# Optimization experiments

Measured on AMD Instinct MI355X. Metric: run time of the kernel, lower is better.

## Reference

```python
import jax, jax.numpy as jnp
import numpy as np

SMOOTH_SIZE = 3      # config.smooth_size (p); window = 2p+1
KERN_LAM = 0.003     # config.kern_lam
# config.kern_smooth = True, config.kern_squash = True, p_dropout = 0 (identity)


def _smooth(k, p):
    # k: (C, L). Reflect-pad then moving average with window 2p+1 (conv1d with ones/W).
    w = 2 * p + 1
    kp = jnp.pad(k, ((0, 0), (p, p)), mode="reflect")            # (C, L+2p)
    smooth_w = jnp.ones((1, 1, w), dtype=k.dtype) / w            # (out=1, in=1, W)
    out = jax.lax.conv_general_dilated(kp[:, None, :], smooth_w,
                                       window_strides=(1,), padding="VALID")
    return out[:, 0, :]                                          # (C, L)


def _squash(k, lam):
    # soft-threshold: relu(|k| - lam) * sign(k)
    return jax.nn.relu(jnp.abs(k) - lam) * jnp.sign(k)


def _fftconv(x, k):
    # x: (B, C, L), k: (C, L) -> causal-ish linear conv via zero-padded FFT, truncated to L
    L = x.shape[-1]
    xf = jnp.fft.rfft(x, n=2 * L)                                # (B, C, L+1) complex
    kf = jnp.fft.rfft(k, n=2 * L)                                # (C, L+1) complex, broadcasts
    return jnp.fft.irfft(xf * kf, n=2 * L)[..., :L]              # (B, C, L)


def setup_inputs() -> dict:
    key = jax.random.key(0)
    kx, kk = jax.random.split(key)
    x = jax.random.normal(kx, (8, 256, 8192), dtype=jnp.float32)
    kern = jax.random.normal(kk, (256, 8192), dtype=jnp.float32) * 0.02
    return {"x": x, "kern": kern}


def reference(x, kern):
    k = _smooth(kern, SMOOTH_SIZE)
    k = _squash(k, KERN_LAM)
    # dropout with p=0 is identity
    return _fftconv(x, k)
```

## Files before the change

kernel.cpp:

```cpp
#include <hip/hip_runtime.h>
#include <math.h>

#define L_SEQ    8192
#define NFFT     8192
#define LOG2N    13
#define NTHREADS 512
#define NB       8
#define NC       256
#define PI_F     3.14159265358979323846f

__device__ __forceinline__ float2 cmul(float2 a, float2 b) {
    return make_float2(fmaf(a.x, b.x, -(a.y * b.y)), fmaf(a.x, b.y, a.y * b.x));
}
__device__ __forceinline__ float2 cadd(float2 a, float2 b) { return make_float2(a.x + b.x, a.y + b.y); }
__device__ __forceinline__ float2 csub(float2 a, float2 b) { return make_float2(a.x - b.x, a.y - b.y); }
__device__ __forceinline__ float2 conj2(float2 a) { return make_float2(a.x, -a.y); }
__device__ __forceinline__ int brev13(unsigned x) { return (int)(__brev(x) >> (32 - LOG2N)); }

__device__ __forceinline__ void fft_dif(float2* z, const int tid) {
    for (int m = NFFT / 2; m >= 1; m >>= 1) {
        __syncthreads();
        const float ang = -PI_F / (float)m;
        #pragma unroll
        for (int r = 0; r < (NFFT / 2) / NTHREADS; ++r) {
            const int k  = r * NTHREADS + tid;
            const int j  = k & (m - 1);
            const int i0 = 2 * k - j;
            const int i1 = i0 + m;
            const float2 a = z[i0];
            const float2 b = z[i1];
            float s, cc;
            __sincosf(ang * (float)j, &s, &cc);
            z[i0] = cadd(a, b);
            z[i1] = cmul(csub(a, b), make_float2(cc, s));
        }
    }
    __syncthreads();
}

__device__ __forceinline__ void fft_dit_inv(float2* z, const int tid) {
    for (int m = 1; m <= NFFT / 2; m <<= 1) {
        __syncthreads();
        const float ang = PI_F / (float)m;
        #pragma unroll
        for (int r = 0; r < (NFFT / 2) / NTHREADS; ++r) {
            const int k  = r * NTHREADS + tid;
            const int j  = k & (m - 1);
            const int i0 = 2 * k - j;
            const int i1 = i0 + m;
            const float2 a = z[i0];
            float s, cc;
            __sincosf(ang * (float)j, &s, &cc);
            const float2 b = cmul(z[i1], make_float2(cc, s));
            z[i0] = cadd(a, b);
            z[i1] = csub(a, b);
        }
    }
    __syncthreads();
}

__global__ __launch_bounds__(NTHREADS)
void fftconv_kernel(const float* __restrict__ x,
                    const float* __restrict__ kern,
                    float* __restrict__ out) {
    extern __shared__ float2 z[];
    const int tid = threadIdx.x;
    const int c   = blockIdx.x >> 1;
    const int bh  = blockIdx.x & 1;

    {
        const float* kr = kern + (size_t)c * L_SEQ;
        const int base = tid * 16;
        float v[16];
        #pragma unroll
        for (int e = 0; e < 16; ++e) {
            const int i = base + e;
            float s = 0.f;
            #pragma unroll
            for (int d = -3; d <= 3; ++d) {
                int idx = i + d;
                idx = (idx < 0) ? -idx : idx;
                idx = (idx >= L_SEQ) ? (2 * L_SEQ - 2 - idx) : idx;
                s += kr[idx];
            }
            s *= (1.0f / 7.0f);
            const float a = fabsf(s) - 0.003f;
            v[e] = (a > 0.f) ? copysignf(a, s) : 0.f;
        }
        #pragma unroll
        for (int e = 0; e < 8; ++e)
            z[tid * 8 + e] = make_float2(v[2 * e], v[2 * e + 1]);
        #pragma unroll
        for (int r = 0; r < 8; ++r)
            z[NFFT / 2 + r * NTHREADS + tid] = make_float2(0.f, 0.f);
    }
    fft_dif(z, tid);

    float2 kA[9], kB[9];
    #pragma unroll
    for (int it = 0; it < 9; ++it) {
        const int f = tid + it * NTHREADS;
        if (f <= NFFT / 2) {
            const int g = (NFFT - f) & (NFFT - 1);
            const float2 Zf = z[brev13(f)];
            const float2 Zg = z[brev13(g)];
            float s, cc;
            __sincosf(PI_F * (float)f * (1.0f / NFFT), &s, &cc);
            const float2 E = make_float2(0.5f * (Zf.x + Zg.x), 0.5f * (Zf.y - Zg.y));
            const float2 O = make_float2(0.5f * (Zf.y + Zg.y), -0.5f * (Zf.x - Zg.x));
            kA[it] = cadd(E, cmul(make_float2(cc, -s), O));
            kB[it] = cadd(conj2(E), cmul(make_float2(-cc, -s), conj2(O)));
        }
    }

    for (int bi = 0; bi < 4; ++bi) {
        const int b = bh * 4 + bi;
        __syncthreads();
        const float2* xr = (const float2*)(x + ((size_t)b * NC + c) * L_SEQ);
        #pragma unroll
        for (int r = 0; r < 8; ++r)
            z[r * NTHREADS + tid] = xr[r * NTHREADS + tid];
        #pragma unroll
        for (int r = 0; r < 8; ++r)
            z[NFFT / 2 + r * NTHREADS + tid] = make_float2(0.f, 0.f);

        fft_dif(z, tid);

        #pragma unroll
        for (int it = 0; it < 9; ++it) {
            const int f = tid + it * NTHREADS;
            if (f <= NFFT / 2) {
                const int g  = (NFFT - f) & (NFFT - 1);
                const int pf = brev13(f), pg = brev13(g);
                const float2 Zf = z[pf];
                const float2 Zg = z[pg];
                float s, cc;
                __sincosf(PI_F * (float)f * (1.0f / NFFT), &s, &cc);
                const float2 E = make_float2(0.5f * (Zf.x + Zg.x), 0.5f * (Zf.y - Zg.y));
                const float2 O = make_float2(0.5f * (Zf.y + Zg.y), -0.5f * (Zf.x - Zg.x));
                const float2 Xf = cadd(E, cmul(make_float2(cc, -s), O));
                const float2 Xg = cadd(conj2(E), cmul(make_float2(-cc, -s), conj2(O)));
                float2 Yf = cmul(Xf, kA[it]);
                float2 Yg = cmul(Xg, kB[it]);
                Yf = make_float2(Yf.x * (1.0f / NFFT), Yf.y * (1.0f / NFFT));
                Yg = make_float2(Yg.x * (1.0f / NFFT), Yg.y * (1.0f / NFFT));
                const float2 P = make_float2(0.5f * (Yf.x + Yg.x), 0.5f * (Yf.y - Yg.y));
                const float2 Q = make_float2(0.5f * (Yf.x - Yg.x), 0.5f * (Yf.y + Yg.y));
                z[pf] = cadd(P, cmul(make_float2(-s, cc), Q));
                if (f != 0) {
                    const float2 Pg = make_float2(P.x, -P.y);
                    const float2 Qg = make_float2(-Q.x, Q.y);
                    z[pg] = cadd(Pg, cmul(make_float2(-s, -cc), Qg));
                }
            }
        }

        fft_dit_inv(z, tid);

        float2* orow = (float2*)(out + ((size_t)b * NC + c) * L_SEQ);
        #pragma unroll
        for (int r = 0; r < 8; ++r)
            orow[r * NTHREADS + tid] = z[r * NTHREADS + tid];
    }
}

extern "C" void kernel_launch(void* const* d_in, const int* in_sizes, int n_in,
                              void* d_out, int out_size, void* d_ws, size_t ws_size,
                              hipStream_t stream) {
    const float* x    = (const float*)d_in[0];
    const float* kern = (const float*)d_in[1];
    float* out        = (float*)d_out;
    const size_t lds_bytes = (size_t)NFFT * sizeof(float2);
    hipLaunchKernelGGL(fftconv_kernel, dim3(NC * 2), dim3(NTHREADS), lds_bytes, stream,
                       x, kern, out);
}
```

Measured before the change: 378.0 us.

## Replace radix-2 shared-memory FFT with register radix-16 stages and swizzled LDS

Replaces the 13-stage radix-2 LDS FFT, which needs a barrier and a sincos for every stage, with a few register-resident radix-16 passes (16x16x16x2 decomposition). Twiddles come from one sincos per pass plus complex multiplies, LDS indices are XOR-swizzled to avoid bank conflicts, and the last radix-2 step uses cross-lane shuffles. The zero-padded half of the input and the discarded half of the output are skipped in the first and last passes, and the kernel smoothing uses a running sum. Register pressure rises (launch bounds ask for 4 blocks) and the recursive twiddle multiplication may cost some accuracy.

```diff
diff --git a/kernel.cpp b/kernel.cpp
--- a/kernel.cpp
+++ b/kernel.cpp
@@ -1,166 +1,286 @@
 #include <hip/hip_runtime.h>
 #include <math.h>
 
-#define L_SEQ    8192
-#define NFFT     8192
-#define LOG2N    13
-#define NTHREADS 512
-#define NB       8
-#define NC       256
-#define PI_F     3.14159265358979323846f
-
-__device__ __forceinline__ float2 cmul(float2 a, float2 b) {
-    return make_float2(fmaf(a.x, b.x, -(a.y * b.y)), fmaf(a.x, b.y, a.y * b.x));
-}
-__device__ __forceinline__ float2 cadd(float2 a, float2 b) { return make_float2(a.x + b.x, a.y + b.y); }
-__device__ __forceinline__ float2 csub(float2 a, float2 b) { return make_float2(a.x - b.x, a.y - b.y); }
-__device__ __forceinline__ float2 conj2(float2 a) { return make_float2(a.x, -a.y); }
-__device__ __forceinline__ int brev13(unsigned x) { return (int)(__brev(x) >> (32 - LOG2N)); }
-
-__device__ __forceinline__ void fft_dif(float2* z, const int tid) {
-    for (int m = NFFT / 2; m >= 1; m >>= 1) {
-        __syncthreads();
-        const float ang = -PI_F / (float)m;
-        #pragma unroll
-        for (int r = 0; r < (NFFT / 2) / NTHREADS; ++r) {
-            const int k  = r * NTHREADS + tid;
-            const int j  = k & (m - 1);
-            const int i0 = 2 * k - j;
-            const int i1 = i0 + m;
-            const float2 a = z[i0];
-            const float2 b = z[i1];
-            float s, cc;
-            __sincosf(ang * (float)j, &s, &cc);
-            z[i0] = cadd(a, b);
-            z[i1] = cmul(csub(a, b), make_float2(cc, s));
-        }
-    }
-    __syncthreads();
-}
-
-__device__ __forceinline__ void fft_dit_inv(float2* z, const int tid) {
-    for (int m = 1; m <= NFFT / 2; m <<= 1) {
-        __syncthreads();
-        const float ang = PI_F / (float)m;
-        #pragma unroll
-        for (int r = 0; r < (NFFT / 2) / NTHREADS; ++r) {
-            const int k  = r * NTHREADS + tid;
-            const int j  = k & (m - 1);
-            const int i0 = 2 * k - j;
-            const int i1 = i0 + m;
-            const float2 a = z[i0];
-            float s, cc;
-            __sincosf(ang * (float)j, &s, &cc);
-            const float2 b = cmul(z[i1], make_float2(cc, s));
-            z[i0] = cadd(a, b);
-            z[i1] = csub(a, b);
-        }
-    }
-    __syncthreads();
-}
-
-__global__ __launch_bounds__(NTHREADS)
+#define NFFT  8192
+#define L_SEQ 8192
+#define NC    256
+#define NTH   512
+
+typedef float2 cplx;
+
+__device__ __forceinline__ cplx cmul(cplx a, cplx b){
+    return make_float2(fmaf(a.x,b.x,-(a.y*b.y)), fmaf(a.x,b.y,a.y*b.x));
+}
+__device__ __forceinline__ cplx cadd(cplx a, cplx b){ return make_float2(a.x+b.x,a.y+b.y); }
+__device__ __forceinline__ cplx csub(cplx a, cplx b){ return make_float2(a.x-b.x,a.y-b.y); }
+__device__ __forceinline__ int swz(int e){ return e ^ ((e>>4)&15); }
+
+#define C16f 0.9238795325112867f
+#define S16f 0.3826834323650898f
+#define RH   0.7071067811865476f
+#define PI2F 6.28318530717958647692f
+
+template<bool INV>
+__device__ __forceinline__ void radix4(cplx& A0, cplx& A1, cplx& A2, cplx& A3){
+    cplx t0=cadd(A0,A2), t1=csub(A0,A2), t2=cadd(A1,A3), t3=csub(A1,A3);
+    A0=cadd(t0,t2); A2=csub(t0,t2);
+    if(!INV){ A1=make_float2(t1.x+t3.y,t1.y-t3.x); A3=make_float2(t1.x-t3.y,t1.y+t3.x); }
+    else    { A1=make_float2(t1.x-t3.y,t1.y+t3.x); A3=make_float2(t1.x+t3.y,t1.y-t3.x); }
+}
+template<bool INV>
+__device__ __forceinline__ cplx twid(cplx v, float re, float im){
+    return INV ? cmul(v, make_float2(re,  im)) : cmul(v, make_float2(re, -im));
+}
+template<bool INV>
+__device__ __forceinline__ cplx mulmi(cplx v){
+    return INV ? make_float2(-v.y, v.x) : make_float2(v.y, -v.x);
+}
+
+template<bool INV>
+__device__ __forceinline__ void dft16_tail(cplx b[4][4], cplx v[16]){
+    b[1][1]=twid<INV>(b[1][1],C16f,S16f);
+    b[1][2]=twid<INV>(b[1][2],RH,RH);
+    b[1][3]=twid<INV>(b[1][3],S16f,C16f);
+    b[2][1]=twid<INV>(b[2][1],RH,RH);
+    b[2][2]=mulmi<INV>(b[2][2]);
+    b[2][3]=twid<INV>(b[2][3],-RH,RH);
+    b[3][1]=twid<INV>(b[3][1],S16f,C16f);
+    b[3][2]=twid<INV>(b[3][2],-RH,RH);
+    b[3][3]=twid<INV>(b[3][3],-C16f,-S16f);
+    #pragma unroll
+    for(int k0=0;k0<4;k0++){
+        radix4<INV>(b[0][k0],b[1][k0],b[2][k0],b[3][k0]);
+        v[k0]=b[0][k0]; v[k0+4]=b[1][k0]; v[k0+8]=b[2][k0]; v[k0+12]=b[3][k0];
+    }
+}
+template<bool INV>
+__device__ __forceinline__ void dft16(cplx v[16]){
+    cplx b[4][4];
+    #pragma unroll
+    for(int n0=0;n0<4;n0++){
+        b[n0][0]=v[n0]; b[n0][1]=v[n0+4]; b[n0][2]=v[n0+8]; b[n0][3]=v[n0+12];
+        radix4<INV>(b[n0][0],b[n0][1],b[n0][2],b[n0][3]);
+    }
+    dft16_tail<INV>(b, v);
+}
+__device__ __forceinline__ void dft16_half(cplx v[16]){
+    cplx b[4][4];
+    #pragma unroll
+    for(int n0=0;n0<4;n0++){
+        cplx a=v[n0], bb=v[n0+4];
+        b[n0][0]=cadd(a,bb);
+        b[n0][1]=make_float2(a.x+bb.y, a.y-bb.x);
+        b[n0][2]=csub(a,bb);
+        b[n0][3]=make_float2(a.x-bb.y, a.y+bb.x);
+    }
+    dft16_tail<false>(b, v);
+}
+__device__ __forceinline__ void idft16_lo(cplx v[16]){
+    cplx b[4][4];
+    #pragma unroll
+    for(int n0=0;n0<4;n0++){
+        b[n0][0]=v[n0]; b[n0][1]=v[n0+4]; b[n0][2]=v[n0+8]; b[n0][3]=v[n0+12];
+        radix4<true>(b[n0][0],b[n0][1],b[n0][2],b[n0][3]);
+    }
+    b[1][1]=twid<true>(b[1][1],C16f,S16f);
+    b[1][2]=twid<true>(b[1][2],RH,RH);
+    b[1][3]=twid<true>(b[1][3],S16f,C16f);
+    b[2][1]=twid<true>(b[2][1],RH,RH);
+    b[2][2]=mulmi<true>(b[2][2]);
+    b[2][3]=twid<true>(b[2][3],-RH,RH);
+    b[3][1]=twid<true>(b[3][1],S16f,C16f);
+    b[3][2]=twid<true>(b[3][2],-RH,RH);
+    b[3][3]=twid<true>(b[3][3],-C16f,-S16f);
+    #pragma unroll
+    for(int k0=0;k0<4;k0++){
+        cplx a=b[0][k0], bb=b[1][k0], c=b[2][k0], d=b[3][k0];
+        cplx t0=cadd(a,c), t1=csub(a,c), t2=cadd(bb,d), t3=csub(bb,d);
+        v[k0]   = cadd(t0,t2);
+        v[k0+4] = make_float2(t1.x - t3.y, t1.y + t3.x);
+    }
+}
+__device__ __forceinline__ void stwiddle(cplx v[16], float th1){
+    float s,c; __sincosf(th1,&s,&c);
+    cplx w=make_float2(c,s), wm=w;
+    v[1]=cmul(v[1],wm);
+    #pragma unroll
+    for(int m=2;m<16;m++){ wm=cmul(wm,w); v[m]=cmul(v[m],wm); }
+}
+
+template<bool INV>
+__device__ __forceinline__ void stageB(cplx* z, int t){
+    const int q=t&31, bb=t>>5, base=512*bb+q;
+    cplx v[16];
+    #pragma unroll
+    for(int m=0;m<16;m++) v[m]=z[swz(base+32*m)];
+    if(INV){ stwiddle(v,  (PI2F/512.f)*(float)q); dft16<true>(v); }
+    else   { dft16<false>(v); stwiddle(v, -(PI2F/512.f)*(float)q); }
+    #pragma unroll
+    for(int m=0;m<16;m++) z[swz(base+32*m)]=v[m];
+}
+__device__ __forceinline__ void stageCD_fwd(cplx* z, int t){
+    const int q=t&1, bb=t>>1, base=32*bb+q;
+    cplx v[16];
+    #pragma unroll
+    for(int m=0;m<16;m++) v[m]=z[swz(base+2*m)];
+    dft16<false>(v);
+    stwiddle(v, -(PI2F/32.f)*(float)q);
+    const float sg = q ? -1.f : 1.f;
+    #pragma unroll
+    for(int m=0;m<16;m++){
+        float ox=__shfl_xor(v[m].x,1), oy=__shfl_xor(v[m].y,1);
+        v[m]=make_float2(fmaf(sg,v[m].x,ox), fmaf(sg,v[m].y,oy));
+        z[swz(base+2*m)]=v[m];
+    }
+}
+__device__ __forceinline__ void stageDC_inv(cplx* z, int t){
+    const int q=t&1, bb=t>>1, base=32*bb+q;
+    cplx v[16];
+    #pragma unroll
+    for(int m=0;m<16;m++) v[m]=z[swz(base+2*m)];
+    const float sg = q ? -1.f : 1.f;
+    #pragma unroll
+    for(int m=0;m<16;m++){
+        float ox=__shfl_xor(v[m].x,1), oy=__shfl_xor(v[m].y,1);
+        v[m]=make_float2(fmaf(sg,v[m].x,ox), fmaf(sg,v[m].y,oy));
+    }
+    stwiddle(v, (PI2F/32.f)*(float)q);
+    dft16<true>(v);
+    #pragma unroll
+    for(int m=0;m<16;m++) z[swz(base+2*m)]=v[m];
+}
+__device__ __forceinline__ int posf(int f){
+    return 512*(f&15) + 32*((f>>4)&15) + 2*((f>>8)&15) + (f>>12);
+}
+
+__global__ __launch_bounds__(NTH, 4)
 void fftconv_kernel(const float* __restrict__ x,
                     const float* __restrict__ kern,
-                    float* __restrict__ out) {
-    extern __shared__ float2 z[];
-    const int tid = threadIdx.x;
-    const int c   = blockIdx.x >> 1;
-    const int bh  = blockIdx.x & 1;
+                    float* __restrict__ out){
+    extern __shared__ cplx z[];
+    const int t  = threadIdx.x;
+    const int c  = blockIdx.x >> 1;
+    const int bh = blockIdx.x & 1;
+    const int A  = t & 15, B = t >> 4;
 
     {
         const float* kr = kern + (size_t)c * L_SEQ;
-        const int base = tid * 16;
-        float v[16];
-        #pragma unroll
-        for (int e = 0; e < 16; ++e) {
-            const int i = base + e;
-            float s = 0.f;
-            #pragma unroll
-            for (int d = -3; d <= 3; ++d) {
-                int idx = i + d;
-                idx = (idx < 0) ? -idx : idx;
-                idx = (idx >= L_SEQ) ? (2 * L_SEQ - 2 - idx) : idx;
-                s += kr[idx];
-            }
-            s *= (1.0f / 7.0f);
-            const float a = fabsf(s) - 0.003f;
-            v[e] = (a > 0.f) ? copysignf(a, s) : 0.f;
-        }
-        #pragma unroll
-        for (int e = 0; e < 8; ++e)
-            z[tid * 8 + e] = make_float2(v[2 * e], v[2 * e + 1]);
-        #pragma unroll
-        for (int r = 0; r < 8; ++r)
-            z[NFFT / 2 + r * NTHREADS + tid] = make_float2(0.f, 0.f);
-    }
-    fft_dif(z, tid);
-
-    float2 kA[9], kB[9];
-    #pragma unroll
-    for (int it = 0; it < 9; ++it) {
-        const int f = tid + it * NTHREADS;
-        if (f <= NFFT / 2) {
-            const int g = (NFFT - f) & (NFFT - 1);
-            const float2 Zf = z[brev13(f)];
-            const float2 Zg = z[brev13(g)];
-            float s, cc;
-            __sincosf(PI_F * (float)f * (1.0f / NFFT), &s, &cc);
-            const float2 E = make_float2(0.5f * (Zf.x + Zg.x), 0.5f * (Zf.y - Zg.y));
-            const float2 O = make_float2(0.5f * (Zf.y + Zg.y), -0.5f * (Zf.x - Zg.x));
-            kA[it] = cadd(E, cmul(make_float2(cc, -s), O));
-            kB[it] = cadd(conj2(E), cmul(make_float2(-cc, -s), conj2(O)));
-        }
-    }
-
-    for (int bi = 0; bi < 4; ++bi) {
-        const int b = bh * 4 + bi;
-        __syncthreads();
-        const float2* xr = (const float2*)(x + ((size_t)b * NC + c) * L_SEQ);
-        #pragma unroll
-        for (int r = 0; r < 8; ++r)
-            z[r * NTHREADS + tid] = xr[r * NTHREADS + tid];
-        #pragma unroll
-        for (int r = 0; r < 8; ++r)
-            z[NFFT / 2 + r * NTHREADS + tid] = make_float2(0.f, 0.f);
-
-        fft_dif(z, tid);
-
-        #pragma unroll
-        for (int it = 0; it < 9; ++it) {
-            const int f = tid + it * NTHREADS;
-            if (f <= NFFT / 2) {
-                const int g  = (NFFT - f) & (NFFT - 1);
-                const int pf = brev13(f), pg = brev13(g);
-                const float2 Zf = z[pf];
-                const float2 Zg = z[pg];
-                float s, cc;
-                __sincosf(PI_F * (float)f * (1.0f / NFFT), &s, &cc);
-                const float2 E = make_float2(0.5f * (Zf.x + Zg.x), 0.5f * (Zf.y - Zg.y));
-                const float2 O = make_float2(0.5f * (Zf.y + Zg.y), -0.5f * (Zf.x - Zg.x));
-                const float2 Xf = cadd(E, cmul(make_float2(cc, -s), O));
-                const float2 Xg = cadd(conj2(E), cmul(make_float2(-cc, -s), conj2(O)));
-                float2 Yf = cmul(Xf, kA[it]);
-                float2 Yg = cmul(Xg, kB[it]);
-                Yf = make_float2(Yf.x * (1.0f / NFFT), Yf.y * (1.0f / NFFT));
-                Yg = make_float2(Yg.x * (1.0f / NFFT), Yg.y * (1.0f / NFFT));
-                const float2 P = make_float2(0.5f * (Yf.x + Yg.x), 0.5f * (Yf.y - Yg.y));
-                const float2 Q = make_float2(0.5f * (Yf.x - Yg.x), 0.5f * (Yf.y + Yg.y));
-                z[pf] = cadd(P, cmul(make_float2(-s, cc), Q));
-                if (f != 0) {
-                    const float2 Pg = make_float2(P.x, -P.y);
-                    const float2 Qg = make_float2(-Q.x, Q.y);
-                    z[pg] = cadd(Pg, cmul(make_float2(-s, -cc), Qg));
+        float buf[22];
+        #pragma unroll
+        for(int j=0;j<22;j++){
+            int idx = 16*t + j - 3;
+            idx = idx < 0 ? -idx : idx;
+            idx = idx >= L_SEQ ? 2*L_SEQ-2-idx : idx;
+            buf[j] = kr[idx];
+        }
+        float v16[16];
+        float s = buf[0]+buf[1]+buf[2]+buf[3]+buf[4]+buf[5]+buf[6];
+        v16[0]=s;
+        #pragma unroll
+        for(int j=1;j<16;j++){ s += buf[j+6]-buf[j-1]; v16[j]=s; }
+        #pragma unroll
+        for(int j=0;j<16;j++){
+            float sv=v16[j]*(1.f/7.f);
+            float a=fabsf(sv)-0.003f;
+            v16[j]= a>0.f ? copysignf(a,sv) : 0.f;
+        }
+        #pragma unroll
+        for(int e=0;e<8;e++) z[swz(8*t+e)] = make_float2(v16[2*e], v16[2*e+1]);
+    }
+    __syncthreads();
+    {
+        cplx v[16];
+        #pragma unroll
+        for(int m=0;m<8;m++) v[m]=z[swz(t+512*m)];
+        dft16_half(v);
+        stwiddle(v, -(PI2F/8192.f)*(float)t);
+        #pragma unroll
+        for(int m=0;m<16;m++) z[swz(t+512*m)]=v[m];
+    }
+    __syncthreads();
+    stageB<false>(z,t);
+    __syncthreads();
+    stageCD_fwd(z,t);
+    __syncthreads();
+
+    cplx kA[9], kB[9];
+    #pragma unroll
+    for(int it=0; it<9; ++it){
+        const bool act = (it<8) || (t==0);
+        const int f = (it<8) ? (256*A + 8*B + it) : 4096;
+        if(act){
+            const int g  = (NFFT - f) & (NFFT-1);
+            const cplx Zf = z[swz(posf(f))];
+            const cplx Zg = z[swz(posf(g))];
+            float s,cc; __sincosf((PI2F*0.5f/NFFT)*(float)f,&s,&cc);
+            cplx E = make_float2(0.5f*(Zf.x+Zg.x), 0.5f*(Zf.y-Zg.y));
+            cplx O = make_float2(0.5f*(Zf.y+Zg.y), -0.5f*(Zf.x-Zg.x));
+            kA[it] = cadd(E, cmul(make_float2(cc,-s), O));
+            kB[it] = cadd(make_float2(E.x,-E.y), cmul(make_float2(-cc,-s), make_float2(O.x,-O.y)));
+        }
+    }
+
+    for(int bi=0;bi<4;bi++){
+        const int b = bh*4 + bi;
+        __syncthreads();
+        {
+            const cplx* xr = (const cplx*)(x + ((size_t)b*NC + c)*L_SEQ);
+            cplx v[16];
+            #pragma unroll
+            for(int m=0;m<8;m++) v[m]=xr[t+512*m];
+            dft16_half(v);
+            stwiddle(v, -(PI2F/8192.f)*(float)t);
+            #pragma unroll
+            for(int m=0;m<16;m++) z[swz(t+512*m)]=v[m];
+        }
+        __syncthreads();
+        stageB<false>(z,t);
+        __syncthreads();
+        stageCD_fwd(z,t);
+        __syncthreads();
+        #pragma unroll
+        for(int it=0; it<9; ++it){
+            const bool act = (it<8) || (t==0);
+            const int f = (it<8) ? (256*A + 8*B + it) : 4096;
+            if(act){
+                const int g  = (NFFT - f) & (NFFT-1);
+                const int pf = posf(f), pg = posf(g);
+                const cplx Zf = z[swz(pf)];
+                const cplx Zg = z[swz(pg)];
+                float s,cc; __sincosf((PI2F*0.5f/NFFT)*(float)f,&s,&cc);
+                cplx E = make_float2(0.5f*(Zf.x+Zg.x), 0.5f*(Zf.y-Zg.y));
+                cplx O = make_float2(0.5f*(Zf.y+Zg.y), -0.5f*(Zf.x-Zg.x));
+                cplx Xf = cadd(E, cmul(make_float2(cc,-s), O));
+                cplx Xg = cadd(make_float2(E.x,-E.y), cmul(make_float2(-cc,-s), make_float2(O.x,-O.y)));
+                cplx Yf = cmul(Xf, kA[it]);
+                cplx Yg = cmul(Xg, kB[it]);
+                const float inv_n = 1.0f/NFFT;
+                Yf.x*=inv_n; Yf.y*=inv_n; Yg.x*=inv_n; Yg.y*=inv_n;
+                cplx P = make_float2(0.5f*(Yf.x+Yg.x), 0.5f*(Yf.y-Yg.y));
+                cplx Q = make_float2(0.5f*(Yf.x-Yg.x), 0.5f*(Yf.y+Yg.y));
+                z[swz(pf)] = cadd(P, cmul(make_float2(-s,cc),Q));
+                if(f!=0){
+                    cplx Pg = make_float2(P.x,-P.y);
+                    cplx Qg = make_float2(-Q.x,Q.y);
+                    z[swz(pg)] = cadd(Pg, cmul(make_float2(-s,-cc),Qg));
                 }
             }
         }
-
-        fft_dit_inv(z, tid);
-
-        float2* orow = (float2*)(out + ((size_t)b * NC + c) * L_SEQ);
-        #pragma unroll
-        for (int r = 0; r < 8; ++r)
-            orow[r * NTHREADS + tid] = z[r * NTHREADS + tid];
+        __syncthreads();
+        stageDC_inv(z,t);
+        __syncthreads();
+        stageB<true>(z,t);
+        __syncthreads();
+        {
+            cplx v[16];
+            #pragma unroll
+            for(int m=0;m<16;m++) v[m]=z[swz(t+512*m)];
+            stwiddle(v, (PI2F/8192.f)*(float)t);
+            idft16_lo(v);
+            cplx* orow = (cplx*)(out + ((size_t)b*NC + c)*L_SEQ);
+            #pragma unroll
+            for(int m=0;m<8;m++) orow[t+512*m]=v[m];
+        }
     }
 }
 
@@ -170,7 +290,7 @@
     const float* x    = (const float*)d_in[0];
     const float* kern = (const float*)d_in[1];
     float* out        = (float*)d_out;
-    const size_t lds_bytes = (size_t)NFFT * sizeof(float2);
-    hipLaunchKernelGGL(fftconv_kernel, dim3(NC * 2), dim3(NTHREADS), lds_bytes, stream,
+    const size_t lds_bytes = (size_t)NFFT * sizeof(cplx);
+    hipLaunchKernelGGL(fftconv_kernel, dim3(NC*2), dim3(NTH), lds_bytes, stream,
                        x, kern, out);
 }
```

Result: slower. 728.8 us (+92.8%).
